# Kernel tuning notes

Measured on AMD Instinct MI355X. Metric: run time of the kernel, lower is better.

## Reference

```python
import jax, jax.numpy as jnp
import numpy as np

# Module hyperparameters (init_kwargs)
TOP_K = 0.15          # fraction of pixels kept per row when step_percent=1
IGNORE_INDEX = 255

B, K, N, H, W = 8, 3, 8, 384, 384


def setup_inputs() -> dict:
    key = jax.random.key(0)
    k1, k2 = jax.random.split(key)
    # log-probabilities over K classes (nll_loss expects log-probs)
    logits = jax.random.normal(k1, (B, K, N, H, W), dtype=jnp.float32)
    inp = jax.nn.log_softmax(logits, axis=1)
    target = jax.random.randint(k2, (B, N, H, W), 0, K, dtype=jnp.int32)
    return {"input": inp, "target": target, "step_percent": 1}


def reference(input, target, step_percent):
    b, k, n, h, w = input.shape
    P = h * w
    x = input.reshape(b * n, k, P)           # (BN, K, P)
    t = target.reshape(b * n, P)             # (BN, P)

    # per-pixel NLL with ignore_index (ignored pixels contribute 0)
    mask = t != IGNORE_INDEX
    t_safe = jnp.where(mask, t, 0)
    nll = -jnp.take_along_axis(x, t_safe[:, None, :], axis=1)[:, 0, :]  # (BN, P)
    nll = jnp.where(mask, nll, jnp.zeros((), nll.dtype))

    # static k: step_percent is a Python scalar in the original forward
    sp = min(float(step_percent), 1.0)
    n_top_k = int(sp * TOP_K * P + (1.0 - sp) * P)

    top_k_loss, _ = jax.lax.top_k(nll, n_top_k)  # (BN, n_top_k)
    return jnp.mean(top_k_loss)
```

## Files before the change

kernel.cpp:

```cpp
#include <hip/hip_runtime.h>

#define BN      64
#define KCLS    3
#define PPIX    147456
#define NB1     4096
#define NBR     2048
#define BPR     36
#define PXB     4096
#define PXT     16
#define NBLK    (BN * BPR)
#define CANDCAP 2048

static const size_t OFF_BSUM = 0;
static const size_t OFF_BCNT = OFF_BSUM + (size_t)NBLK * 8;
static const size_t OFF_BCC  = OFF_BCNT + (size_t)NBLK * 4;
static const size_t OFF_ACC  = OFF_BCC + (size_t)NBLK * 4;
static const size_t OFF_D2   = OFF_ACC + 8;
static const size_t OFF_CAND = OFF_D2 + 8;

__device__ __forceinline__ unsigned topk_count(const int* sp_ptr) {
    double sp = (double)sp_ptr[0];
    if (sp > 1.0) sp = 1.0;
    return (unsigned)(sp * 0.15 * (double)PPIX + (1.0 - sp) * (double)PPIX);
}

__device__ __forceinline__ float sel_nll(int t, float a, float b, float c) {
    float lp = (t == 0) ? a : ((t == 1) ? b : ((t == 2) ? c : 0.0f));
    return fmaxf(-lp, 0.0f);
}

__global__ __launch_bounds__(256, 4) void k_stream(
    const float* __restrict__ in, const int* __restrict__ tgt, const int* __restrict__ sp,
    double* __restrict__ bsum, unsigned* __restrict__ bcnt, unsigned* __restrict__ bccnt,
    float* __restrict__ cand, double* __restrict__ accum, unsigned* __restrict__ done2)
{
    __shared__ unsigned hist[NB1];
    __shared__ unsigned cred[256];
    __shared__ double   dred[256];
    __shared__ int s_bL, s_bH, lcnt;

    const int tid   = threadIdx.x;
    const int row   = blockIdx.x / BPR;
    const int chunk = blockIdx.x % BPR;

    if (blockIdx.x == 0 && tid == 0) { accum[0] = 0.0; done2[0] = 0u; }

    for (int i = tid; i < NB1; i += 256) hist[i] = 0u;
    if (tid == 0) { s_bL = 0; s_bH = NB1 - 1; lcnt = 0; }
    __syncthreads();

    const float4* p0 = (const float4*)(in + (size_t)row * KCLS * PPIX);
    const float4* p1 = p0 + PPIX / 4;
    const float4* p2 = p1 + PPIX / 4;
    const int4*   t4 = (const int4*)(tgt + (size_t)row * PPIX);
    const int base = chunk * (PXB / 4);

    float v[PXT];
    int idx0 = base + tid;
    int4   T0 = t4[idx0];
    float4 A0 = p0[idx0], B0 = p1[idx0], C0 = p2[idx0];
    #pragma unroll
    for (int b = 0; b < 4; ++b) {
        int4 T1; float4 A1, B1, C1;
        if (b < 3) {
            const int ni = base + (b + 1) * 256 + tid;
            T1 = t4[ni]; A1 = p0[ni]; B1 = p1[ni]; C1 = p2[ni];
        }
        v[4*b+0] = sel_nll(T0.x, A0.x, B0.x, C0.x);
        v[4*b+1] = sel_nll(T0.y, A0.y, B0.y, C0.y);
        v[4*b+2] = sel_nll(T0.z, A0.z, B0.z, C0.z);
        v[4*b+3] = sel_nll(T0.w, A0.w, B0.w, C0.w);
        atomicAdd(&hist[__float_as_uint(v[4*b+0]) >> 19], 1u);
        atomicAdd(&hist[__float_as_uint(v[4*b+1]) >> 19], 1u);
        atomicAdd(&hist[__float_as_uint(v[4*b+2]) >> 19], 1u);
        atomicAdd(&hist[__float_as_uint(v[4*b+3]) >> 19], 1u);
        T0 = T1; A0 = A1; B0 = B1; C0 = C1;
    }
    __syncthreads();

    const unsigned k = topk_count(sp);
    const float p  = (float)k / (float)PPIX;
    const float mu = (float)PXB * p;
    const float sg = sqrtf((float)PXB * p * (1.0f - p));
    const float marg = 10.0f * sg + 8.0f;
    const float tH = mu - marg;
    const float tL = mu + marg;

    unsigned cl[16]; unsigned cacc = 0;
    const int b0 = tid * 16;
    #pragma unroll
    for (int i = 0; i < 16; ++i) {
        cl[i] = hist[NB1 - 1 - (b0 + i)];
        cacc += cl[i];
    }
    cred[tid] = cacc;
    __syncthreads();
    for (int off = 1; off < 256; off <<= 1) {
        unsigned t2 = (tid >= off) ? cred[tid - off] : 0u;
        __syncthreads();
        cred[tid] += t2;
        __syncthreads();
    }
    {
        unsigned cum = tid ? cred[tid - 1] : 0u;
        #pragma unroll
        for (int i = 0; i < 16; ++i) {
            const unsigned cb = cl[i];
            const float fc = (float)cum, fe = (float)(cum + cb);
            if (fc < tH && fe >= tH) s_bH = NB1 - 1 - (b0 + i);
            if (fc < tL && fe >= tL) s_bL = NB1 - 1 - (b0 + i);
            cum += cb;
        }
    }
    __syncthreads();

    const unsigned hi = ((unsigned)s_bH + 1u) << 19;
    const unsigned lo = ((unsigned)s_bL) << 19;
    double acc = 0.0; unsigned cab = 0;
    float* cr = cand + (size_t)blockIdx.x * CANDCAP;
    #pragma unroll
    for (int i = 0; i < PXT; ++i) {
        const unsigned u = __float_as_uint(v[i]);
        if (u >= hi) {
            acc += (double)v[i]; ++cab;
        } else if (u >= lo) {
            const int pos = atomicAdd(&lcnt, 1);
            if (pos < CANDCAP) cr[pos] = v[i];
        }
    }
    dred[tid] = acc; cred[tid] = cab;
    __syncthreads();
    for (int s = 128; s > 0; s >>= 1) {
        if (tid < s) { dred[tid] += dred[tid + s]; cred[tid] += cred[tid + s]; }
        __syncthreads();
    }
    if (tid == 0) {
        bsum[blockIdx.x]  = dred[0];
        bcnt[blockIdx.x]  = cred[0];
        bccnt[blockIdx.x] = (unsigned)((lcnt > CANDCAP) ? CANDCAP : lcnt);
    }
}

__global__ __launch_bounds__(256) void k_resolve(
    const float* __restrict__ cand, const unsigned* __restrict__ bccnt,
    const unsigned* __restrict__ bcnt, const double* __restrict__ bsum,
    const int* __restrict__ sp, double* __restrict__ accum,
    unsigned* __restrict__ done2, float* __restrict__ out)
{
    __shared__ unsigned hc[NBR];
    __shared__ unsigned cred[256];
    __shared__ double   dred[256];
    __shared__ int s_t, s_r;

    const int row = blockIdx.x, tid = threadIdx.x;
    const unsigned k = topk_count(sp);

    {
        double a = 0.0; unsigned c = 0;
        for (int s = tid; s < BPR; s += 256) {
            a += bsum[row * BPR + s];
            c += bcnt[row * BPR + s];
        }
        dred[tid] = a; cred[tid] = c;
        __syncthreads();
        for (int s = 128; s > 0; s >>= 1) {
            if (tid < s) { dred[tid] += dred[tid + s]; cred[tid] += cred[tid + s]; }
            __syncthreads();
        }
    }
    const double S = dred[0];
    const unsigned above = cred[0];
    long rr = (long)k - (long)above;
    if (rr < 1) rr = 1;
    __syncthreads();

    unsigned clo = 0u, cbhi = 0x80000000u;
    for (;;) {
        const unsigned width = cbhi - clo;
        const bool exact = (width <= (unsigned)NBR);
        int s2 = 0;
        if (!exact) {
            const unsigned w1 = width - 1u;
            const int m = 32 - __clz((int)w1);
            s2 = m - 11;
        }
        for (int i = tid; i < NBR; i += 256) hc[i] = 0u;
        __syncthreads();
        for (int seg = 0; seg < BPR; ++seg) {
            const int bi = row * BPR + seg;
            const int sn = (int)bccnt[bi];
            const float* sv = cand + (size_t)bi * CANDCAP;
            for (int i = tid; i < sn; i += 256) {
                const unsigned u = __float_as_uint(sv[i]);
                if (u >= clo && u < cbhi) atomicAdd(&hc[(u - clo) >> s2], 1u);
            }
        }
        __syncthreads();

        unsigned cl[8]; unsigned cacc = 0;
        const int b0 = tid * 8;
        #pragma unroll
        for (int i = 0; i < 8; ++i) { cl[i] = hc[NBR - 1 - (b0 + i)]; cacc += cl[i]; }
        cred[tid] = cacc;
        __syncthreads();
        for (int off = 1; off < 256; off <<= 1) {
            unsigned t2 = (tid >= off) ? cred[tid - off] : 0u;
            __syncthreads();
            cred[tid] += t2;
            __syncthreads();
        }
        long cum = tid ? (long)cred[tid - 1] : 0;
        #pragma unroll
        for (int i = 0; i < 8; ++i) {
            const long cb = (long)cl[i];
            if (cum < rr && cum + cb >= rr) {
                s_t = NBR - 1 - (b0 + i);
                s_r = (int)(rr - cum);
            }
            cum += cb;
        }
        __syncthreads();
        if (exact) break;
        const unsigned nlo = clo + ((unsigned)s_t << s2);
        unsigned nhi = nlo + (1u << s2);
        if (nhi > cbhi) nhi = cbhi;
        clo = nlo; cbhi = nhi;
        rr = s_r;
        __syncthreads();
    }

    const unsigned tbits = clo + (unsigned)s_t;
    double acc = 0.0;
    for (int seg = 0; seg < BPR; ++seg) {
        const int bi = row * BPR + seg;
        const int sn = (int)bccnt[bi];
        const float* sv = cand + (size_t)bi * CANDCAP;
        for (int i = tid; i < sn; i += 256) {
            const float x = sv[i];
            if (__float_as_uint(x) > tbits) acc += (double)x;
        }
    }
    dred[tid] = acc;
    __syncthreads();
    for (int s = 128; s > 0; s >>= 1) {
        if (tid < s) dred[tid] += dred[tid + s];
        __syncthreads();
    }

    if (tid == 0) {
        const double total = S + dred[0] + (double)s_r * (double)__uint_as_float(tbits);
        atomicAdd(accum, total);
        __threadfence();
        const unsigned o2 = atomicAdd(done2, 1u);
        if (o2 == BN - 1) {
            __threadfence();
            const double a = atomicAdd(accum, 0.0);
            out[0] = (float)(a / ((double)BN * (double)k));
        }
    }
}

extern "C" void kernel_launch(void* const* d_in, const int* in_sizes, int n_in,
                              void* d_out, int out_size, void* d_ws, size_t ws_size,
                              hipStream_t stream)
{
    const float* in  = (const float*)d_in[0];
    const int*   tgt = (const int*)d_in[1];
    const int*   sp  = (const int*)d_in[2];

    char* ws = (char*)d_ws;
    double*   bsum  = (double*)(ws + OFF_BSUM);
    unsigned* bcnt  = (unsigned*)(ws + OFF_BCNT);
    unsigned* bccnt = (unsigned*)(ws + OFF_BCC);
    double*   accum = (double*)(ws + OFF_ACC);
    unsigned* done2 = (unsigned*)(ws + OFF_D2);
    float*    cand  = (float*)(ws + OFF_CAND);

    k_stream <<<NBLK, 256, 0, stream>>>(in, tgt, sp, bsum, bcnt, bccnt, cand, accum, done2);
    k_resolve<<<BN, 256, 0, stream>>>(cand, bccnt, bcnt, bsum, sp, accum, done2, (float*)d_out);
}
```

Before: 287.0 us.

## Batch loads upfront, flatten candidate segments, and narrow radix range via min/max

In the first kernel, all sixteen vector loads per thread are issued together before compute, and histogram atomics are grouped afterwards, replacing the one-step software prefetch. The resolve kernel builds a prefix over per-segment candidate counts so threads iterate over a flat index space instead of looping per segment with poor occupancy. It also computes the min and max candidate bits so the radix refinement starts from a narrow range, which should need fewer passes. The costs are a binary search per candidate access, extra reductions, and higher register pressure from holding all loads.

```diff
diff --git a/kernel.cpp b/kernel.cpp
--- a/kernel.cpp
+++ b/kernel.cpp
@@ -55,27 +55,26 @@
     const int4*   t4 = (const int4*)(tgt + (size_t)row * PPIX);
     const int base = chunk * (PXB / 4);
 
+    int4   T[4]; float4 A[4], B[4], C[4];
+    #pragma unroll
+    for (int b = 0; b < 4; ++b) T[b] = t4[base + b * 256 + tid];
+    #pragma unroll
+    for (int b = 0; b < 4; ++b) A[b] = p0[base + b * 256 + tid];
+    #pragma unroll
+    for (int b = 0; b < 4; ++b) B[b] = p1[base + b * 256 + tid];
+    #pragma unroll
+    for (int b = 0; b < 4; ++b) C[b] = p2[base + b * 256 + tid];
+
     float v[PXT];
-    int idx0 = base + tid;
-    int4   T0 = t4[idx0];
-    float4 A0 = p0[idx0], B0 = p1[idx0], C0 = p2[idx0];
     #pragma unroll
     for (int b = 0; b < 4; ++b) {
-        int4 T1; float4 A1, B1, C1;
-        if (b < 3) {
-            const int ni = base + (b + 1) * 256 + tid;
-            T1 = t4[ni]; A1 = p0[ni]; B1 = p1[ni]; C1 = p2[ni];
-        }
-        v[4*b+0] = sel_nll(T0.x, A0.x, B0.x, C0.x);
-        v[4*b+1] = sel_nll(T0.y, A0.y, B0.y, C0.y);
-        v[4*b+2] = sel_nll(T0.z, A0.z, B0.z, C0.z);
-        v[4*b+3] = sel_nll(T0.w, A0.w, B0.w, C0.w);
-        atomicAdd(&hist[__float_as_uint(v[4*b+0]) >> 19], 1u);
-        atomicAdd(&hist[__float_as_uint(v[4*b+1]) >> 19], 1u);
-        atomicAdd(&hist[__float_as_uint(v[4*b+2]) >> 19], 1u);
-        atomicAdd(&hist[__float_as_uint(v[4*b+3]) >> 19], 1u);
-        T0 = T1; A0 = A1; B0 = B1; C0 = C1;
-    }
+        v[4*b+0] = sel_nll(T[b].x, A[b].x, B[b].x, C[b].x);
+        v[4*b+1] = sel_nll(T[b].y, A[b].y, B[b].y, C[b].y);
+        v[4*b+2] = sel_nll(T[b].z, A[b].z, B[b].z, C[b].z);
+        v[4*b+3] = sel_nll(T[b].w, A[b].w, B[b].w, C[b].w);
+    }
+    #pragma unroll
+    for (int i = 0; i < PXT; ++i) atomicAdd(&hist[__float_as_uint(v[i]) >> 19], 1u);
     __syncthreads();
 
     const unsigned k = topk_count(sp);
@@ -150,7 +149,8 @@
     __shared__ unsigned hc[NBR];
     __shared__ unsigned cred[256];
     __shared__ double   dred[256];
-    __shared__ int s_t, s_r;
+    __shared__ int  pseg[BPR + 1];
+    __shared__ int  s_t, s_r;
 
     const int row = blockIdx.x, tid = threadIdx.x;
     const unsigned k = topk_count(sp);
@@ -167,89 +167,124 @@
             if (tid < s) { dred[tid] += dred[tid + s]; cred[tid] += cred[tid + s]; }
             __syncthreads();
         }
+        if (tid == 0) {
+            int run = 0;
+            pseg[0] = 0;
+            for (int s = 0; s < BPR; ++s) { run += (int)bccnt[row * BPR + s]; pseg[s + 1] = run; }
+        }
+        __syncthreads();
     }
     const double S = dred[0];
     const unsigned above = cred[0];
+    const int n = pseg[BPR];
     long rr = (long)k - (long)above;
     if (rr < 1) rr = 1;
-    __syncthreads();
-
-    unsigned clo = 0u, cbhi = 0x80000000u;
-    for (;;) {
-        const unsigned width = cbhi - clo;
-        const bool exact = (width <= (unsigned)NBR);
-        int s2 = 0;
-        if (!exact) {
-            const unsigned w1 = width - 1u;
-            const int m = 32 - __clz((int)w1);
-            s2 = m - 11;
-        }
-        for (int i = tid; i < NBR; i += 256) hc[i] = 0u;
-        __syncthreads();
-        for (int seg = 0; seg < BPR; ++seg) {
-            const int bi = row * BPR + seg;
-            const int sn = (int)bccnt[bi];
-            const float* sv = cand + (size_t)bi * CANDCAP;
-            for (int i = tid; i < sn; i += 256) {
-                const unsigned u = __float_as_uint(sv[i]);
+    if (rr > n) rr = n;
+    __syncthreads();
+
+    const float* crow = cand + (size_t)row * BPR * CANDCAP;
+    #define CAND_AT(g, dst) {                                              \
+        int lo_ = 0, hi_ = BPR;                                            \
+        while (hi_ - lo_ > 1) { int m_ = (lo_ + hi_) >> 1;                 \
+            if ((g) >= pseg[m_]) lo_ = m_; else hi_ = m_; }                \
+        dst = crow[(size_t)lo_ * CANDCAP + ((g) - pseg[lo_])]; }
+
+    double tail = 0.0;
+    if (n > 0) {
+        unsigned umin = 0xFFFFFFFFu, umax = 0u;
+        for (int g = tid; g < n; g += 256) {
+            float x; CAND_AT(g, x);
+            const unsigned u = __float_as_uint(x);
+            umin = (u < umin) ? u : umin;
+            umax = (u > umax) ? u : umax;
+        }
+        cred[tid] = umin;
+        __syncthreads();
+        for (int s = 128; s > 0; s >>= 1) {
+            if (tid < s) { const unsigned o = cred[tid + s]; if (o < cred[tid]) cred[tid] = o; }
+            __syncthreads();
+        }
+        umin = cred[0];
+        __syncthreads();
+        cred[tid] = umax;
+        __syncthreads();
+        for (int s = 128; s > 0; s >>= 1) {
+            if (tid < s) { const unsigned o = cred[tid + s]; if (o > cred[tid]) cred[tid] = o; }
+            __syncthreads();
+        }
+        umax = cred[0];
+        __syncthreads();
+
+        unsigned clo = umin, cbhi = umax + 1u;
+        for (;;) {
+            const unsigned width = cbhi - clo;
+            const bool exact = (width <= (unsigned)NBR);
+            int s2 = 0;
+            if (!exact) {
+                const unsigned w1 = width - 1u;
+                const int m = 32 - __clz((int)w1);
+                s2 = m - 11;
+            }
+            for (int i = tid; i < NBR; i += 256) hc[i] = 0u;
+            __syncthreads();
+            for (int g = tid; g < n; g += 256) {
+                float x; CAND_AT(g, x);
+                const unsigned u = __float_as_uint(x);
                 if (u >= clo && u < cbhi) atomicAdd(&hc[(u - clo) >> s2], 1u);
             }
-        }
-        __syncthreads();
-
-        unsigned cl[8]; unsigned cacc = 0;
-        const int b0 = tid * 8;
-        #pragma unroll
-        for (int i = 0; i < 8; ++i) { cl[i] = hc[NBR - 1 - (b0 + i)]; cacc += cl[i]; }
-        cred[tid] = cacc;
-        __syncthreads();
-        for (int off = 1; off < 256; off <<= 1) {
-            unsigned t2 = (tid >= off) ? cred[tid - off] : 0u;
-            __syncthreads();
-            cred[tid] += t2;
-            __syncthreads();
-        }
-        long cum = tid ? (long)cred[tid - 1] : 0;
-        #pragma unroll
-        for (int i = 0; i < 8; ++i) {
-            const long cb = (long)cl[i];
-            if (cum < rr && cum + cb >= rr) {
-                s_t = NBR - 1 - (b0 + i);
-                s_r = (int)(rr - cum);
+            __syncthreads();
+
+            unsigned cl[8]; unsigned cacc = 0;
+            const int b0 = tid * 8;
+            #pragma unroll
+            for (int i = 0; i < 8; ++i) { cl[i] = hc[NBR - 1 - (b0 + i)]; cacc += cl[i]; }
+            cred[tid] = cacc;
+            __syncthreads();
+            for (int off = 1; off < 256; off <<= 1) {
+                unsigned t2 = (tid >= off) ? cred[tid - off] : 0u;
+                __syncthreads();
+                cred[tid] += t2;
+                __syncthreads();
             }
-            cum += cb;
-        }
-        __syncthreads();
-        if (exact) break;
-        const unsigned nlo = clo + ((unsigned)s_t << s2);
-        unsigned nhi = nlo + (1u << s2);
-        if (nhi > cbhi) nhi = cbhi;
-        clo = nlo; cbhi = nhi;
-        rr = s_r;
-        __syncthreads();
-    }
-
-    const unsigned tbits = clo + (unsigned)s_t;
-    double acc = 0.0;
-    for (int seg = 0; seg < BPR; ++seg) {
-        const int bi = row * BPR + seg;
-        const int sn = (int)bccnt[bi];
-        const float* sv = cand + (size_t)bi * CANDCAP;
-        for (int i = tid; i < sn; i += 256) {
-            const float x = sv[i];
+            long cum = tid ? (long)cred[tid - 1] : 0;
+            #pragma unroll
+            for (int i = 0; i < 8; ++i) {
+                const long cb = (long)cl[i];
+                if (cum < rr && cum + cb >= rr) {
+                    s_t = NBR - 1 - (b0 + i);
+                    s_r = (int)(rr - cum);
+                }
+                cum += cb;
+            }
+            __syncthreads();
+            if (exact) break;
+            const unsigned nlo = clo + ((unsigned)s_t << s2);
+            unsigned nhi = nlo + (1u << s2);
+            if (nhi > cbhi) nhi = cbhi;
+            clo = nlo; cbhi = nhi;
+            rr = s_r;
+            __syncthreads();
+        }
+
+        const unsigned tbits = clo + (unsigned)s_t;
+        double acc = 0.0;
+        for (int g = tid; g < n; g += 256) {
+            float x; CAND_AT(g, x);
             if (__float_as_uint(x) > tbits) acc += (double)x;
         }
-    }
-    dred[tid] = acc;
-    __syncthreads();
-    for (int s = 128; s > 0; s >>= 1) {
-        if (tid < s) dred[tid] += dred[tid + s];
-        __syncthreads();
-    }
+        dred[tid] = acc;
+        __syncthreads();
+        for (int s = 128; s > 0; s >>= 1) {
+            if (tid < s) dred[tid] += dred[tid + s];
+            __syncthreads();
+        }
+        if (tid == 0)
+            tail = dred[0] + (double)s_r * (double)__uint_as_float(tbits);
+    }
+    #undef CAND_AT
 
     if (tid == 0) {
-        const double total = S + dred[0] + (double)s_r * (double)__uint_as_float(tbits);
-        atomicAdd(accum, total);
+        atomicAdd(accum, S + tail);
         __threadfence();
         const unsigned o2 = atomicAdd(done2, 1u);
         if (o2 == BN - 1) {
```

Result: slower. 381.4 us (+32.9%).
